# Optimization experiments

Hardware: AMD Instinct MI355X
Metric: run time of the kernel (lower is better)

## Reference

```python
import jax, jax.numpy as jnp
import numpy as np

# Straight-through binarization: forward hard threshold, backward identity.
# Matches BinarizeTensorThresh / BinarizedLinearFunction / BinaryActivation STE
# semantics from the diffnaps my_layers module (grad_weight = g^T x, i.e. the
# continuous weight receives the gradient of the binary weight unchanged).

def make_ste(thresh):
    @jax.custom_vjp
    def f(x):
        return (x >= thresh).astype(x.dtype)
    def fwd(x):
        return f(x), None
    def bwd(_, g):
        return (g,)
    f.defvjp(fwd, bwd)
    return f

ste_half = make_ste(0.5)  # weight binarization threshold (the 0.5 ctor arg)
ste_one = make_ste(1.0)   # activation fires when (pre-act + bias) >= 1

B, D, H, L = 4096, 5000, 2000, 50  # batch, input_dim(items), hidden_dim(patterns), label_dim
DATA_SPARSITY = 0.05


def setup_inputs() -> dict:
    key = jax.random.key(0)
    k = jax.random.split(key, 5)
    # sparse binary transaction data
    x = (jax.random.uniform(k[0], (B, D)) < DATA_SPARSITY).astype(jnp.float32)
    # continuous encoder weight in [0,1); binarized at 0.5 inside forward
    W_enc = jax.random.uniform(k[1], (H, D), dtype=jnp.float32)
    # small negative encoder bias (BinaPs-style init)
    b_enc = -jnp.abs(jax.random.normal(k[2], (H,), dtype=jnp.float32)) * 0.1
    act0_bias = jnp.zeros((H,), jnp.float32)
    act3_bias = jnp.zeros((D,), jnp.float32)
    # classifier_weight = logit(clip(N(0.1, 0.1), 0.01, 0.99)) as in __init__
    y = jnp.clip(0.1 + 0.1 * jax.random.normal(k[3], (L, H), dtype=jnp.float32), 0.01, 0.99)
    classifier_weight = jnp.log(y / (1.0 - y))
    return {
        "x": x,
        "W_enc": W_enc,
        "b_enc": b_enc,
        "act0_bias": act0_bias,
        "act3_bias": act3_bias,
        "classifier_weight": classifier_weight,
    }


def reference(x, W_enc, b_enc, act0_bias, act3_bias, classifier_weight):
    # fc0_enc: binarized-weight linear with bias
    Wb = ste_half(W_enc)                       # [H, D] in {0,1}
    h = x @ Wb.T + b_enc                       # [B, H]
    # act0: binary activation (threshold 1 on biased pre-activation)
    z = ste_one(h + act0_bias)                 # [B, H]
    # classify: sigmoid-gated classifier head (external_classifier=None / mode 'None')
    final_w = jax.nn.sigmoid(classifier_weight / 0.5)  # [L, H]
    classification = z @ final_w.T             # [B, L]
    # fc3_dec: shares the binarized encoder weight, transposed, no bias
    xd = z @ Wb                                # [B, D]
    output = ste_one(xd + act3_bias)           # [B, D]
    return output, classification, z
```

## Files before the change

kernel.cpp:

```cpp
#include <hip/hip_runtime.h>
#include <stdint.h>

static constexpr int Bn = 4096;
static constexpr int Dn = 5000;
static constexpr int Hn = 2000;
static constexpr int Ln = 50;
static constexpr int XW = 80;
static constexpr int Hpad = 2048;
static constexpr int Dpad = 5120;

typedef int v4i __attribute__((ext_vector_type(4)));
typedef int v16i __attribute__((ext_vector_type(16)));

#if defined(__has_builtin)
#if __has_builtin(__builtin_amdgcn_global_load_lds)
#define HAVE_GLOAD_LDS 1
#endif
#endif

#ifdef HAVE_GLOAD_LDS
__device__ __forceinline__ void gload16(const uint8_t* g, uint8_t* l) {
  __builtin_amdgcn_global_load_lds(
      (const __attribute__((address_space(1))) uint32_t*)g,
      (__attribute__((address_space(3))) uint32_t*)l, 16, 0, 0);
}
#endif

__device__ __forceinline__ int popc_acc(uint64_t v, int acc) {
  acc = __builtin_popcount((uint32_t)v) + acc;
  acc = __builtin_popcount((uint32_t)(v >> 32)) + acc;
  return acc;
}

__global__ void k_pack_i8(const float* __restrict__ src, uint8_t* __restrict__ dst,
                          int nrows_out, int nrows_valid, int ncols_src) {
  int g = (int)blockIdx.x * 256 + (int)threadIdx.x;
  int row = g / (Dpad / 4);
  int c4 = g - row * (Dpad / 4);
  if (row >= nrows_out) return;
  int col = c4 * 4;
  uchar4 o = make_uchar4(0, 0, 0, 0);
  if (row < nrows_valid && col + 3 < ncols_src) {
    const float4 v = *(const float4*)(src + (size_t)row * ncols_src + col);
    o.x = v.x >= 0.5f; o.y = v.y >= 0.5f; o.z = v.z >= 0.5f; o.w = v.w >= 0.5f;
  }
  *(uchar4*)(dst + (size_t)row * Dpad + col) = o;
}

__global__ __launch_bounds__(256) void k_pack_w_dual(const float* __restrict__ W,
                                                     uint8_t* __restrict__ wi8,
                                                     uint8_t* __restrict__ wtd) {
  int d = (int)blockIdx.x * 256 + (int)threadIdx.x;
  int j0 = (int)blockIdx.y * 64;
  bool dv = d < Dn;
  uint64_t colbits = 0;
  for (int r = 0; r < 64; ++r) {
    int j = j0 + r;
    float v = (j < Hn && dv) ? W[(size_t)j * Dn + d] : 0.0f;
    uint8_t bit = (v >= 0.5f) ? 1 : 0;
    wi8[(size_t)j * Dpad + d] = bit;
    colbits |= ((uint64_t)bit) << r;
  }
  uint8_t* dst = wtd + (size_t)d * Hpad + j0;
#pragma unroll
  for (int q = 0; q < 4; ++q) {
    uint32_t u[4];
#pragma unroll
    for (int s = 0; s < 4; ++s) {
      uint32_t nib = (uint32_t)((colbits >> (q * 16 + s * 4)) & 0xFull);
      u[s] = (nib & 1u) | (((nib >> 1) & 1u) << 8) | (((nib >> 2) & 1u) << 16) |
             (((nib >> 3) & 1u) << 24);
    }
    *(uint4*)(dst + q * 16) = make_uint4(u[0], u[1], u[2], u[3]);
  }
}

__global__ void k_pack_x(const float* __restrict__ x, uint64_t* __restrict__ xb2) {
  int g = (int)((blockIdx.x * blockDim.x + threadIdx.x) >> 6);
  int lane = (int)(threadIdx.x & 63);
  constexpr int nq = XW >> 2;
  int row = g / nq;
  int q = g - row * nq;
  if (row >= Bn) return;
  int w0 = q << 2;
  unsigned long long m[4];
#pragma unroll
  for (int e = 0; e < 4; ++e) {
    int col = ((w0 + e) << 6) + lane;
    float v = (col < Dn) ? x[(size_t)row * Dn + col] : 0.0f;
    m[e] = __ballot(v >= 0.5f);
  }
  if (lane < 4) {
    unsigned long long mv = m[0];
    mv = (lane == 1) ? m[1] : mv;
    mv = (lane == 2) ? m[2] : mv;
    mv = (lane == 3) ? m[3] : mv;
    int w = w0 + lane;
    xb2[((size_t)(w >> 1) * Bn + row) * 2 + (w & 1)] = mv;
  }
}

__global__ void k_pack_w(const float* __restrict__ W, uint64_t* __restrict__ wbT) {
  int g = (int)((blockIdx.x * blockDim.x + threadIdx.x) >> 6);
  int lane = (int)(threadIdx.x & 63);
  constexpr int nq = XW >> 2;
  int row = g / nq;
  int q = g - row * nq;
  if (row >= Hn) return;
  int w0 = q << 2;
  unsigned long long m[4];
#pragma unroll
  for (int e = 0; e < 4; ++e) {
    int col = ((w0 + e) << 6) + lane;
    float v = (col < Dn) ? W[(size_t)row * Dn + col] : 0.0f;
    m[e] = __ballot(v >= 0.5f);
  }
  if (lane < 4) {
    unsigned long long mv = m[0];
    mv = (lane == 1) ? m[1] : mv;
    mv = (lane == 2) ? m[2] : mv;
    mv = (lane == 3) ? m[3] : mv;
    wbT[(size_t)(w0 + lane) * Hpad + row] = mv;
  }
}

__global__ void k_transp(const uint64_t* __restrict__ wbT, uint32_t* __restrict__ wt32) {
  int g = (int)((blockIdx.x * blockDim.x + threadIdx.x) >> 6);
  int lane = (int)(threadIdx.x & 63);
  int w = g % XW;
  int jc = g / XW;
  if (jc >= Hpad / 64) return;
  uint64_t word = wbT[(size_t)w * Hpad + jc * 64 + lane];
  uint64_t mym = 0;
#pragma unroll
  for (int e = 0; e < 64; ++e) {
    unsigned long long m = __ballot((word >> e) & 1ull);
    mym = (lane == e) ? m : mym;
  }
  int d = w * 64 + lane;
  wt32[(size_t)(jc * 2) * Dpad + d] = (uint32_t)mym;
  wt32[(size_t)(jc * 2 + 1) * Dpad + d] = (uint32_t)(mym >> 32);
}

__global__ void k_pack_fwT(const float* __restrict__ cw, float* __restrict__ fwT) {
  int idx = blockIdx.x * blockDim.x + threadIdx.x;
  if (idx >= Hn * 64) return;
  int j = idx >> 6, l = idx & 63;
  float v = 0.0f;
  if (l < Ln) {
    float t = 2.0f * cw[(size_t)l * Hn + j];
    v = 1.0f / (1.0f + expf(-t));
  }
  fwT[idx] = v;
}

__global__ void k_zero(float* __restrict__ p, int n) {
  int i = blockIdx.x * blockDim.x + threadIdx.x;
  if (i < n) p[i] = 0.0f;
}


#ifdef HAVE_GLOAD_LDS
#define GEMM_PIPE(LDK, NT, Abase, Bbase)                                        \
  int srow_l = lane >> 2;                                           \
  int scol = (((lane & 3) ^ ((lane >> 3) & 3)) << 4);                          \
  const uint8_t* aSrc[2];                                                      \
  const uint8_t* bSrc[2];                                                      \
  uint8_t* asd[2][2];                                                          \
  uint8_t* bsd[2][2];                                                          \
  _Pragma("unroll") for (int i = 0; i < 2; ++i) {                              \
    int rbaseS = wv * 32 + i * 16;                                             \
    aSrc[i] = (Abase) + (size_t)(bm * 128 + rbaseS + srow_l) * (LDK) + scol;   \
    bSrc[i] = (Bbase) + (size_t)(bn * 128 + rbaseS + srow_l) * (LDK) + scol;   \
    asd[0][i] = As + rbaseS * 64;                                              \
    asd[1][i] = As + 8192 + rbaseS * 64;                                       \
    bsd[0][i] = Bs + rbaseS * 64;                                              \
    bsd[1][i] = Bs + 8192 + rbaseS * 64;                                       \
  }                                                                            \
  int arow = wm * 64 + (lane & 31);                                            \
  int brow = wn * 64 + (lane & 31);                                            \
  int khalf = lane >> 5;                                                       \
  int asl = (arow >> 1) & 3;                                                   \
  int bsl = (brow >> 1) & 3;                                                   \
                                                                 \
  _Pragma("unroll") for (int i = 0; i < 2; ++i) {                              \
    gload16(aSrc[i], asd[0][i]);                                               \
    gload16(bSrc[i], bsd[0][i]);                                               \
  }                                                                            \
  __syncthreads();                                                             \
  _Pragma("unroll 1") for (int t = 0; t < (NT); ++t) {                         \
    int cur = t & 1;                                                           \
    if (t + 1 < (NT)) {                                                        \
      size_t koff = (size_t)(t + 1) * 64;                                      \
      _Pragma("unroll") for (int i = 0; i < 2; ++i) {                          \
        gload16(aSrc[i] + koff, asd[cur ^ 1][i]);                              \
        gload16(bSrc[i] + koff, bsd[cur ^ 1][i]);                              \
      }                                                                        \
    }                                                                          \
    const uint8_t* Ab = As + cur * 8192;                                       \
    const uint8_t* Bb = Bs + cur * 8192;                                       \
    _Pragma("unroll") for (int kk = 0; kk < 2; ++kk) {                         \
      int kq = kk * 2 + khalf;                                                 \
      v4i a0 = *(const v4i*)(Ab + arow * 64 + ((kq ^ asl) << 4));              \
      v4i a1 = *(const v4i*)(Ab + (arow + 32) * 64 + ((kq ^ asl) << 4));       \
      v4i b0 = *(const v4i*)(Bb + brow * 64 + ((kq ^ bsl) << 4));              \
      v4i b1 = *(const v4i*)(Bb + (brow + 32) * 64 + ((kq ^ bsl) << 4));       \
      acc[0][0] = __builtin_amdgcn_mfma_i32_32x32x32_i8(a0, b0, acc[0][0], 0, 0, 0); \
      acc[0][1] = __builtin_amdgcn_mfma_i32_32x32x32_i8(a0, b1, acc[0][1], 0, 0, 0); \
      acc[1][0] = __builtin_amdgcn_mfma_i32_32x32x32_i8(a1, b0, acc[1][0], 0, 0, 0); \
      acc[1][1] = __builtin_amdgcn_mfma_i32_32x32x32_i8(a1, b1, acc[1][1], 0, 0, 0); \
    }                                                                          \
    __syncthreads();                                                           \
  }
#else
#define GEMM_PIPE(LDK, NT, Abase, Bbase)                                       \
  int srow_l = tid >> 2;                                            \
  int sq = tid & 3;                                                            \
  const uint8_t* ap0 = (Abase) + (size_t)(bm * 128 + srow_l) * (LDK) + sq * 16;\
  const uint8_t* ap1 = ap0 + (size_t)64 * (LDK);                               \
  const uint8_t* bp0 = (Bbase) + (size_t)(bn * 128 + srow_l) * (LDK) + sq * 16;\
  const uint8_t* bp1 = bp0 + (size_t)64 * (LDK);                               \
  int lw0 = srow_l * 64 + ((sq ^ ((srow_l >> 1) & 3)) << 4);                   \
  int lw1 = (64 + srow_l) * 64 + ((sq ^ (((64 + srow_l) >> 1) & 3)) << 4);     \
  int arow = wm * 64 + (lane & 31);                                            \
  int brow = wn * 64 + (lane & 31);                                            \
  int khalf = lane >> 5;                                                       \
  int asl = (arow >> 1) & 3;                                                   \
  int bsl = (brow >> 1) & 3;                                                   \
  _Pragma("unroll 1") for (int t = 0; t < (NT); ++t) {                         \
    size_t koff = (size_t)t * 64;                                              \
    v4i ra0 = *(const v4i*)(ap0 + koff);                                       \
    v4i ra1 = *(const v4i*)(ap1 + koff);                                       \
    v4i rb0 = *(const v4i*)(bp0 + koff);                                       \
    v4i rb1 = *(const v4i*)(bp1 + koff);                                       \
    __syncthreads();                                                           \
    *(v4i*)(As + lw0) = ra0;                                                   \
    *(v4i*)(As + lw1) = ra1;                                                   \
    *(v4i*)(Bs + lw0) = rb0;                                                   \
    *(v4i*)(Bs + lw1) = rb1;                                                   \
    __syncthreads();                                                           \
    _Pragma("unroll") for (int kk = 0; kk < 2; ++kk) {                         \
      int kq = kk * 2 + khalf;                                                 \
      v4i a0 = *(const v4i*)(As + arow * 64 + ((kq ^ asl) << 4));              \
      v4i a1 = *(const v4i*)(As + (arow + 32) * 64 + ((kq ^ asl) << 4));       \
      v4i b0 = *(const v4i*)(Bs + brow * 64 + ((kq ^ bsl) << 4));              \
      v4i b1 = *(const v4i*)(Bs + (brow + 32) * 64 + ((kq ^ bsl) << 4));       \
      acc[0][0] = __builtin_amdgcn_mfma_i32_32x32x32_i8(a0, b0, acc[0][0], 0, 0, 0); \
      acc[0][1] = __builtin_amdgcn_mfma_i32_32x32x32_i8(a0, b1, acc[0][1], 0, 0, 0); \
      acc[1][0] = __builtin_amdgcn_mfma_i32_32x32x32_i8(a1, b0, acc[1][0], 0, 0, 0); \
      acc[1][1] = __builtin_amdgcn_mfma_i32_32x32x32_i8(a1, b1, acc[1][1], 0, 0, 0); \
    }                                                                          \
  }
#endif

__global__ __launch_bounds__(256) void k_enc_mfma(
    const uint8_t* __restrict__ A, const uint8_t* __restrict__ B,
    const float* __restrict__ b_enc, const float* __restrict__ act0b,
    float* __restrict__ z_out, uint8_t* __restrict__ zi8) {
#ifdef HAVE_GLOAD_LDS
  __shared__ uint8_t As[2 * 128 * 64];
  __shared__ uint8_t Bs[2 * 128 * 64];
#else
  __shared__ uint8_t As[128 * 64];
  __shared__ uint8_t Bs[128 * 64];
#endif
  int tid = (int)threadIdx.x;
  int bn = (int)blockIdx.x;
  int bm = (int)blockIdx.y;
  int wv = __builtin_amdgcn_readfirstlane(tid >> 6);
  int lane = tid & 63;
  int wm = wv >> 1, wn = wv & 1;

  v16i acc[2][2];
#pragma unroll
  for (int i = 0; i < 2; ++i)
#pragma unroll
    for (int j = 0; j < 2; ++j) acc[i][j] = (v16i)0;

  GEMM_PIPE(Dpad, Dpad / 64, A, B)

  int col0 = bn * 128 + wn * 64 + (lane & 31);
#pragma unroll
  for (int ni = 0; ni < 2; ++ni) {
    int j = col0 + ni * 32;
    int js = (j < Hn) ? j : (Hn - 1);
    float be = b_enc[js];
    float ab = act0b[js];
    bool jv = j < Hn;
#pragma unroll
    for (int mi = 0; mi < 2; ++mi) {
      int rbase = bm * 128 + wm * 64 + mi * 32;
#pragma unroll
      for (int r = 0; r < 16; ++r) {
        int rloc = (r & 3) + 8 * (r >> 2) + 4 * (lane >> 5);
        int b = rbase + rloc;
        float h = ((float)acc[mi][ni][r] + be) + ab;
        bool zb = jv && (h >= 1.0f);
        if (jv) {
          z_out[(size_t)b * Hn + j] = zb ? 1.0f : 0.0f;
          zi8[(size_t)b * Hpad + j] = zb ? 1 : 0;
        }
      }
    }
  }
}

__global__ __launch_bounds__(256) void k_dec_mfma(
    const uint8_t* __restrict__ A,
    const uint8_t* __restrict__ B,
    const float* __restrict__ act3b, float* __restrict__ out) {
#ifdef HAVE_GLOAD_LDS
  __shared__ uint8_t As[2 * 128 * 64];
  __shared__ uint8_t Bs[2 * 128 * 64];
#else
  __shared__ uint8_t As[128 * 64];
  __shared__ uint8_t Bs[128 * 64];
#endif
  int tid = (int)threadIdx.x;
  int bn = (int)blockIdx.x;
  int bm = (int)blockIdx.y;
  int wv = __builtin_amdgcn_readfirstlane(tid >> 6);
  int lane = tid & 63;
  int wm = wv >> 1, wn = wv & 1;

  v16i acc[2][2];
#pragma unroll
  for (int i = 0; i < 2; ++i)
#pragma unroll
    for (int j = 0; j < 2; ++j) acc[i][j] = (v16i)0;

  GEMM_PIPE(Hpad, Hpad / 64, A, B)

  int col0 = bn * 128 + wn * 64 + (lane & 31);
#pragma unroll
  for (int ni = 0; ni < 2; ++ni) {
    int d = col0 + ni * 32;
    int ds = (d < Dn) ? d : (Dn - 1);
    float ab = act3b[ds];
    bool dv = d < Dn;
#pragma unroll
    for (int mi = 0; mi < 2; ++mi) {
      int rbase = bm * 128 + wm * 64 + mi * 32;
#pragma unroll
      for (int r = 0; r < 16; ++r) {
        int rloc = (r & 3) + 8 * (r >> 2) + 4 * (lane >> 5);
        int b = rbase + rloc;
        if (dv) out[(size_t)b * Dn + d] = (((float)acc[mi][ni][r] + ab) >= 1.0f) ? 1.0f : 0.0f;
      }
    }
  }
}

__global__ __launch_bounds__(256) void k_enc_bit(const uint64_t* __restrict__ xb2,
                                                 const uint64_t* __restrict__ wbT,
                                                 const float* __restrict__ b_enc,
                                                 const float* __restrict__ act0b,
                                                 float* __restrict__ z_out,
                                                 uint8_t* __restrict__ zb8) {
  __shared__ uint64_t wl[XW][8];
  int tid = (int)threadIdx.x;
  int jg = (int)blockIdx.x;
  int j0 = jg << 3;
#pragma unroll
  for (int k = 0; k < 3; ++k) {
    int idx = k * 256 + tid;
    if (idx < XW * 8) {
      int w = idx >> 3, j = idx & 7;
      wl[w][j] = wbT[(size_t)w * Hpad + j0 + j];
    }
  }
  __syncthreads();
  int wv = __builtin_amdgcn_readfirstlane(tid >> 6);
  int lane = tid & 63;
  int bg = (int)blockIdx.y * 4 + wv;
  int b0 = (bg << 8) + lane;
  int acc[4][8] = {};
  const uint64_t* xp = xb2 + 2 * (size_t)b0;
#pragma unroll 1
  for (int w2 = 0; w2 < XW / 2; ++w2) {
    ulong2 xx[4];
#pragma unroll
    for (int i = 0; i < 4; ++i)
      xx[i] = *(const ulong2*)(xp + ((size_t)w2 * Bn + i * 64) * 2);
#pragma unroll
    for (int t2 = 0; t2 < 4; ++t2) {
      ulong2 wa = *(ulong2*)&wl[2 * w2][2 * t2];
      ulong2 wb = *(ulong2*)&wl[2 * w2 + 1][2 * t2];
#pragma unroll
      for (int i = 0; i < 4; ++i) {
        acc[i][2 * t2]     = popc_acc(xx[i].x & wa.x, acc[i][2 * t2]);
        acc[i][2 * t2 + 1] = popc_acc(xx[i].x & wa.y, acc[i][2 * t2 + 1]);
        acc[i][2 * t2]     = popc_acc(xx[i].y & wb.x, acc[i][2 * t2]);
        acc[i][2 * t2 + 1] = popc_acc(xx[i].y & wb.y, acc[i][2 * t2 + 1]);
      }
    }
  }
  float be[8], ab[8];
#pragma unroll
  for (int t = 0; t < 8; ++t) {
    int j = j0 + t;
    int js = (j < Hn) ? j : (Hn - 1);
    be[t] = b_enc[js];
    ab[t] = act0b[js];
  }
#pragma unroll
  for (int i = 0; i < 4; ++i) {
    int b = b0 + i * 64;
    uint32_t zbyte = 0;
    float zf[8];
#pragma unroll
    for (int t = 0; t < 8; ++t) {
      int j = j0 + t;
      float h = ((float)acc[i][t] + be[t]) + ab[t];
      bool zb = (j < Hn) && (h >= 1.0f);
      zbyte |= zb ? (1u << t) : 0u;
      zf[t] = zb ? 1.0f : 0.0f;
    }
    zb8[((size_t)(jg >> 2) * Bn + b) * 4 + (jg & 3)] = (uint8_t)zbyte;
    if (j0 < Hn) {
      float* zp = z_out + (size_t)b * Hn + j0;
      *(float4*)zp = make_float4(zf[0], zf[1], zf[2], zf[3]);
      *(float4*)(zp + 4) = make_float4(zf[4], zf[5], zf[6], zf[7]);
    }
  }
}

__global__ __launch_bounds__(256, 6) void k_dec_bit(const uint32_t* __restrict__ zb32,
                                                    const uint32_t* __restrict__ wt32,
                                                    const float* __restrict__ act3b,
                                                    float* __restrict__ out) {
  __shared__ uint32_t tl[64][8];
  int tid = (int)threadIdx.x;
  int dc = (int)blockIdx.x;
  int d0 = dc << 3;
  {
#pragma unroll
    for (int k = 0; k < 2; ++k) {
      int e = k * 256 + tid;
      int hw = e >> 3, dl = e & 7;
      tl[hw][dl] = wt32[(size_t)hw * Dpad + d0 + dl];
    }
  }
  __syncthreads();
  int wv = __builtin_amdgcn_readfirstlane(tid >> 6);
  int lane = tid & 63;
  int bg = (int)blockIdx.y * 4 + wv;
  int b0 = (bg << 8) + lane;
  int acc[4][8] = {};
  const uint32_t* zp = zb32 + b0;
  uint32_t z0, z1, z2, z3, n0, n1, n2, n3;
  uint4 wA, wB, wAn, wBn;
  z0 = zp[0]; z1 = zp[64]; z2 = zp[128]; z3 = zp[192];
  wA = *(const uint4*)&tl[0][0];
  wB = *(const uint4*)&tl[0][4];
#define DEC_MAC()                                          \
  do {                                                     \
    acc[0][0] = __builtin_popcount(z0 & wA.x) + acc[0][0]; \
    acc[0][1] = __builtin_popcount(z0 & wA.y) + acc[0][1]; \
    acc[0][2] = __builtin_popcount(z0 & wA.z) + acc[0][2]; \
    acc[0][3] = __builtin_popcount(z0 & wA.w) + acc[0][3]; \
    acc[0][4] = __builtin_popcount(z0 & wB.x) + acc[0][4]; \
    acc[0][5] = __builtin_popcount(z0 & wB.y) + acc[0][5]; \
    acc[0][6] = __builtin_popcount(z0 & wB.z) + acc[0][6]; \
    acc[0][7] = __builtin_popcount(z0 & wB.w) + acc[0][7]; \
    acc[1][0] = __builtin_popcount(z1 & wA.x) + acc[1][0]; \
    acc[1][1] = __builtin_popcount(z1 & wA.y) + acc[1][1]; \
    acc[1][2] = __builtin_popcount(z1 & wA.z) + acc[1][2]; \
    acc[1][3] = __builtin_popcount(z1 & wA.w) + acc[1][3]; \
    acc[1][4] = __builtin_popcount(z1 & wB.x) + acc[1][4]; \
    acc[1][5] = __builtin_popcount(z1 & wB.y) + acc[1][5]; \
    acc[1][6] = __builtin_popcount(z1 & wB.z) + acc[1][6]; \
    acc[1][7] = __builtin_popcount(z1 & wB.w) + acc[1][7]; \
    acc[2][0] = __builtin_popcount(z2 & wA.x) + acc[2][0]; \
    acc[2][1] = __builtin_popcount(z2 & wA.y) + acc[2][1]; \
    acc[2][2] = __builtin_popcount(z2 & wA.z) + acc[2][2]; \
    acc[2][3] = __builtin_popcount(z2 & wA.w) + acc[2][3]; \
    acc[2][4] = __builtin_popcount(z2 & wB.x) + acc[2][4]; \
    acc[2][5] = __builtin_popcount(z2 & wB.y) + acc[2][5]; \
    acc[2][6] = __builtin_popcount(z2 & wB.z) + acc[2][6]; \
    acc[2][7] = __builtin_popcount(z2 & wB.w) + acc[2][7]; \
    acc[3][0] = __builtin_popcount(z3 & wA.x) + acc[3][0]; \
    acc[3][1] = __builtin_popcount(z3 & wA.y) + acc[3][1]; \
    acc[3][2] = __builtin_popcount(z3 & wA.z) + acc[3][2]; \
    acc[3][3] = __builtin_popcount(z3 & wA.w) + acc[3][3]; \
    acc[3][4] = __builtin_popcount(z3 & wB.x) + acc[3][4]; \
    acc[3][5] = __builtin_popcount(z3 & wB.y) + acc[3][5]; \
    acc[3][6] = __builtin_popcount(z3 & wB.z) + acc[3][6]; \
    acc[3][7] = __builtin_popcount(z3 & wB.w) + acc[3][7]; \
  } while (0)
#pragma unroll 1
  for (int hw = 0; hw < 64; ++hw) {
    int hn = (hw < 63) ? hw + 1 : hw;
    const uint32_t* zq = zp + (size_t)hn * Bn;
    n0 = zq[0]; n1 = zq[64]; n2 = zq[128]; n3 = zq[192];
    wAn = *(const uint4*)&tl[hn][0];
    wBn = *(const uint4*)&tl[hn][4];
    DEC_MAC();
    z0 = n0; z1 = n1; z2 = n2; z3 = n3;
    wA = wAn; wB = wBn;
  }
#undef DEC_MAC
  float ab[8];
#pragma unroll
  for (int t = 0; t < 8; ++t) {
    int d = d0 + t;
    int ds = (d < Dn) ? d : (Dn - 1);
    ab[t] = act3b[ds];
  }
  if (d0 < Dn) {
#pragma unroll
    for (int i = 0; i < 4; ++i) {
      int b = b0 + i * 64;
      float of[8];
#pragma unroll
      for (int t = 0; t < 8; ++t)
        of[t] = (((float)acc[i][t] + ab[t]) >= 1.0f) ? 1.0f : 0.0f;
      float* op = out + (size_t)b * Dn + d0;
      *(float4*)op = make_float4(of[0], of[1], of[2], of[3]);
      *(float4*)(op + 4) = make_float4(of[4], of[5], of[6], of[7]);
    }
  }
}

__global__ __launch_bounds__(256) void k_cls_i8(const uint8_t* __restrict__ zi8,
                                                const float* __restrict__ fwT,
                                                float* __restrict__ cls) {
  __shared__ float zT[64][132];
  __shared__ float fwL[64][64];
  int tid = (int)threadIdx.x;
  int bb0 = (int)blockIdx.x * 128;
  int jsp = (int)blockIdx.y;
  int tx = tid & 15, ty = tid >> 4;
  float acc[8][4] = {};
  for (int tile = 0; tile < 4; ++tile) {
    int jt0 = jsp * 256 + tile * 64;
    __syncthreads();
#pragma unroll
    for (int k = 0; k < 8; ++k) {
      int idx = k * 256 + tid;
      int r = idx >> 4, c4 = idx & 15;
      int j = jt0 + c4 * 4;
      uchar4 v = make_uchar4(0, 0, 0, 0);
      if (j < Hn) v = *(const uchar4*)(zi8 + (size_t)(bb0 + r) * Hpad + j);
      zT[c4 * 4 + 0][r] = (float)v.x;
      zT[c4 * 4 + 1][r] = (float)v.y;
      zT[c4 * 4 + 2][r] = (float)v.z;
      zT[c4 * 4 + 3][r] = (float)v.w;
    }
#pragma unroll
    for (int k = 0; k < 4; ++k) {
      int idx = k * 256 + tid;
      int jj = idx >> 4, c4 = idx & 15;
      int j = jt0 + jj;
      float4 v = make_float4(0.f, 0.f, 0.f, 0.f);
      if (j < Hn) v = *(const float4*)(fwT + (size_t)j * 64 + c4 * 4);
      *(float4*)&fwL[jj][c4 * 4] = v;
    }
    __syncthreads();
#pragma unroll 4
    for (int jj = 0; jj < 64; ++jj) {
      float4 fv = *(float4*)&fwL[jj][tx * 4];
      float4 za = *(float4*)&zT[jj][ty * 8];
      float4 zb = *(float4*)&zT[jj][ty * 8 + 4];
      float zz[8] = {za.x, za.y, za.z, za.w, zb.x, zb.y, zb.z, zb.w};
      float ff[4] = {fv.x, fv.y, fv.z, fv.w};
#pragma unroll
      for (int i = 0; i < 8; ++i)
#pragma unroll
        for (int l = 0; l < 4; ++l) acc[i][l] += zz[i] * ff[l];
    }
  }
#pragma unroll
  for (int i = 0; i < 8; ++i) {
    int b = bb0 + ty * 8 + i;
#pragma unroll
    for (int l = 0; l < 4; ++l) {
      int L = tx * 4 + l;
      if (L < Ln) atomicAdd(&cls[(size_t)b * Ln + L], acc[i][l]);
    }
  }
}

__global__ __launch_bounds__(256) void k_cls_f32(const float* __restrict__ z,
                                                 const float* __restrict__ fwT,
                                                 float* __restrict__ cls) {
  __shared__ float zT[64][132];
  __shared__ float fwL[64][64];
  int tid = (int)threadIdx.x;
  int bb0 = (int)blockIdx.x * 128;
  int jsp = (int)blockIdx.y;
  int tx = tid & 15, ty = tid >> 4;
  float acc[8][4] = {};
  for (int tile = 0; tile < 4; ++tile) {
    int jt0 = jsp * 256 + tile * 64;
    __syncthreads();
#pragma unroll
    for (int k = 0; k < 8; ++k) {
      int idx = k * 256 + tid;
      int r = idx >> 4, c4 = idx & 15;
      int j = jt0 + c4 * 4;
      float4 v = make_float4(0.f, 0.f, 0.f, 0.f);
      if (j < Hn) v = *(const float4*)(z + (size_t)(bb0 + r) * Hn + j);
      zT[c4 * 4 + 0][r] = v.x;
      zT[c4 * 4 + 1][r] = v.y;
      zT[c4 * 4 + 2][r] = v.z;
      zT[c4 * 4 + 3][r] = v.w;
    }
#pragma unroll
    for (int k = 0; k < 4; ++k) {
      int idx = k * 256 + tid;
      int jj = idx >> 4, c4 = idx & 15;
      int j = jt0 + jj;
      float4 v = make_float4(0.f, 0.f, 0.f, 0.f);
      if (j < Hn) v = *(const float4*)(fwT + (size_t)j * 64 + c4 * 4);
      *(float4*)&fwL[jj][c4 * 4] = v;
    }
    __syncthreads();
#pragma unroll 4
    for (int jj = 0; jj < 64; ++jj) {
      float4 fv = *(float4*)&fwL[jj][tx * 4];
      float4 za = *(float4*)&zT[jj][ty * 8];
      float4 zb = *(float4*)&zT[jj][ty * 8 + 4];
      float zz[8] = {za.x, za.y, za.z, za.w, zb.x, zb.y, zb.z, zb.w};
      float ff[4] = {fv.x, fv.y, fv.z, fv.w};
#pragma unroll
      for (int i = 0; i < 8; ++i)
#pragma unroll
        for (int l = 0; l < 4; ++l) acc[i][l] += zz[i] * ff[l];
    }
  }
#pragma unroll
  for (int i = 0; i < 8; ++i) {
    int b = bb0 + ty * 8 + i;
#pragma unroll
    for (int l = 0; l < 4; ++l) {
      int L = tx * 4 + l;
      if (L < Ln) atomicAdd(&cls[(size_t)b * Ln + L], acc[i][l]);
    }
  }
}

extern "C" void kernel_launch(void* const* d_in, const int* in_sizes, int n_in,
                              void* d_out, int out_size, void* d_ws, size_t ws_size,
                              hipStream_t stream) {
  const float* x     = (const float*)d_in[0];
  const float* W     = (const float*)d_in[1];
  const float* b_enc = (const float*)d_in[2];
  const float* act0b = (const float*)d_in[3];
  const float* act3b = (const float*)d_in[4];
  const float* cw    = (const float*)d_in[5];

  float* out0 = (float*)d_out;
  float* cls  = out0 + (size_t)Bn * Dn;
  float* zout = cls + (size_t)Bn * Ln;

  char* p = (char*)d_ws;
  uint32_t* zb32 = (uint32_t*)p; p += (size_t)64 * Bn * 4;
  float*    fwT  = (float*)p;    p += (size_t)Hn * 64 * 4;
  size_t common = (size_t)(p - (char*)d_ws);

  size_t sz_xi8 = (size_t)Bn * Dpad;
  size_t sz_wi8 = (size_t)Hpad * Dpad;
  size_t sz_zi8 = (size_t)Bn * Hpad;
  size_t sz_wtd = (size_t)Dpad * Hpad;
  size_t sz_wbT = (size_t)XW * Hpad * 8;
  size_t sz_wt32 = (size_t)64 * Dpad * 4;
  size_t full_need = common + sz_xi8 + sz_wi8 + sz_zi8 + sz_wtd;

  k_pack_fwT<<<(Hn * 64 + 255) / 256, 256, 0, stream>>>(cw, fwT);
  k_zero<<<(Bn * Ln + 255) / 256, 256, 0, stream>>>(cls, Bn * Ln);

  if (ws_size >= full_need) {
    uint8_t* xi8 = (uint8_t*)p;
    uint8_t* wi8 = xi8 + sz_xi8;
    uint8_t* zi8 = wi8 + sz_wi8;
    uint8_t* wtd = zi8 + sz_zi8;
    k_pack_i8<<<(Bn * (Dpad / 4) + 255) / 256, 256, 0, stream>>>(x, xi8, Bn, Bn, Dn);
    dim3 gwd(Dpad / 256, Hpad / 64);
    k_pack_w_dual<<<gwd, 256, 0, stream>>>(W, wi8, wtd);
    dim3 ge(Hpad / 128, Bn / 128);
    k_enc_mfma<<<ge, 256, 0, stream>>>(xi8, wi8, b_enc, act0b, zout, zi8);
    dim3 g3(32, 8);
    k_cls_i8<<<g3, 256, 0, stream>>>(zi8, fwT, cls);
    dim3 gd(Dpad / 128, Bn / 128);
    k_dec_mfma<<<gd, 256, 0, stream>>>(zi8, wtd, act3b, out0);
  } else {
    uint64_t* wbT  = (uint64_t*)p;
    uint32_t* wt32 = (uint32_t*)(p + sz_wbT);
    uint64_t* xb2  = (uint64_t*)(p + sz_wbT + sz_wt32);
    {
      long long waves = (long long)Hn * (XW / 4);
      k_pack_w<<<(int)((waves * 64 + 255) / 256), 256, 0, stream>>>(W, wbT);
    }
    {
      long long waves = (long long)(Hpad / 64) * XW;
      k_transp<<<(int)((waves * 64 + 255) / 256), 256, 0, stream>>>(wbT, wt32);
    }
    {
      long long waves = (long long)Bn * (XW / 4);
      k_pack_x<<<(int)((waves * 64 + 255) / 256), 256, 0, stream>>>(x, xb2);
    }
    dim3 g1(256, 4);
    k_enc_bit<<<g1, 256, 0, stream>>>(xb2, wbT, b_enc, act0b, zout, (uint8_t*)zb32);
    dim3 g3(32, 8);
    k_cls_f32<<<g3, 256, 0, stream>>>(zout, fwT, cls);
    dim3 g2(640, 4);
    k_dec_bit<<<g2, 256, 0, stream>>>(zb32, wt32, act3b, out0);
  }
}
```

Before: 246.0 us.

## Store int8 operands in k-blocked 16-byte layout and deepen GEMM k-tile to 128

```diff
diff --git a/kernel.cpp b/kernel.cpp
--- a/kernel.cpp
+++ b/kernel.cpp
@@ -32,36 +32,47 @@
   return acc;
 }
 
-__global__ void k_pack_i8(const float* __restrict__ src, uint8_t* __restrict__ dst,
-                          int nrows_out, int nrows_valid, int ncols_src) {
+__global__ void k_pack_xT(const float* __restrict__ x, uint8_t* __restrict__ xiT) {
   int g = (int)blockIdx.x * 256 + (int)threadIdx.x;
-  int row = g / (Dpad / 4);
-  int c4 = g - row * (Dpad / 4);
-  if (row >= nrows_out) return;
-  int col = c4 * 4;
-  uchar4 o = make_uchar4(0, 0, 0, 0);
-  if (row < nrows_valid && col + 3 < ncols_src) {
-    const float4 v = *(const float4*)(src + (size_t)row * ncols_src + col);
-    o.x = v.x >= 0.5f; o.y = v.y >= 0.5f; o.z = v.z >= 0.5f; o.w = v.w >= 0.5f;
-  }
-  *(uchar4*)(dst + (size_t)row * Dpad + col) = o;
-}
-
-__global__ __launch_bounds__(256) void k_pack_w_dual(const float* __restrict__ W,
-                                                     uint8_t* __restrict__ wi8,
-                                                     uint8_t* __restrict__ wtd) {
+  int kb = g >> 12;
+  int row = g & 4095;
+  if (kb >= Dpad / 16) return;
+  uint8_t o[16];
+  int c0 = kb * 16;
+  if (c0 + 15 < Dn) {
+#pragma unroll
+    for (int q = 0; q < 4; ++q) {
+      float4 v = *(const float4*)(x + (size_t)row * Dn + c0 + q * 4);
+      o[q * 4 + 0] = v.x >= 0.5f;
+      o[q * 4 + 1] = v.y >= 0.5f;
+      o[q * 4 + 2] = v.z >= 0.5f;
+      o[q * 4 + 3] = v.w >= 0.5f;
+    }
+  } else {
+#pragma unroll
+    for (int e = 0; e < 16; ++e) {
+      int c = c0 + e;
+      o[e] = (c < Dn) ? (x[(size_t)row * Dn + c] >= 0.5f ? 1 : 0) : 0;
+    }
+  }
+  *(uint4*)(xiT + ((size_t)kb * Bn + row) * 16) = *(uint4*)o;
+}
+
+__global__ __launch_bounds__(256) void k_pack_w_dualT(const float* __restrict__ W,
+                                                      uint8_t* __restrict__ wi8T,
+                                                      uint8_t* __restrict__ wtdT) {
   int d = (int)blockIdx.x * 256 + (int)threadIdx.x;
   int j0 = (int)blockIdx.y * 64;
   bool dv = d < Dn;
+  int dc = d >> 4, de = d & 15;
   uint64_t colbits = 0;
   for (int r = 0; r < 64; ++r) {
     int j = j0 + r;
     float v = (j < Hn && dv) ? W[(size_t)j * Dn + d] : 0.0f;
     uint8_t bit = (v >= 0.5f) ? 1 : 0;
-    wi8[(size_t)j * Dpad + d] = bit;
+    wi8T[((size_t)dc * Hpad + j) * 16 + de] = bit;
     colbits |= ((uint64_t)bit) << r;
   }
-  uint8_t* dst = wtd + (size_t)d * Hpad + j0;
 #pragma unroll
   for (int q = 0; q < 4; ++q) {
     uint32_t u[4];
@@ -71,7 +82,8 @@
       u[s] = (nib & 1u) | (((nib >> 1) & 1u) << 8) | (((nib >> 2) & 1u) << 16) |
              (((nib >> 3) & 1u) << 24);
     }
-    *(uint4*)(dst + q * 16) = make_uint4(u[0], u[1], u[2], u[3]);
+    *(uint4*)(wtdT + (((size_t)(j0 >> 4) + q) * Dpad + d) * 16) =
+        make_uint4(u[0], u[1], u[2], u[3]);
   }
 }
 
@@ -161,50 +173,42 @@
 
 
 #ifdef HAVE_GLOAD_LDS
-#define GEMM_PIPE(LDK, NT, Abase, Bbase)                                        \
-  int srow_l = lane >> 2;                                           \
-  int scol = (((lane & 3) ^ ((lane >> 3) & 3)) << 4);                          \
-  const uint8_t* aSrc[2];                                                      \
-  const uint8_t* bSrc[2];                                                      \
-  uint8_t* asd[2][2];                                                          \
-  uint8_t* bsd[2][2];                                                          \
+#define GEMM_PIPE(AROWS, BROWS, NT, Abase, Bbase)                               \
+  const uint8_t* aS = (Abase) + ((size_t)bm * 128 + lane) * 16;                \
+  const uint8_t* bS = (Bbase) + ((size_t)bn * 128 + lane) * 16;                \
+  int kqw = 2 * wv;                           \
   _Pragma("unroll") for (int i = 0; i < 2; ++i) {                              \
-    int rbaseS = wv * 32 + i * 16;                                             \
-    aSrc[i] = (Abase) + (size_t)(bm * 128 + rbaseS + srow_l) * (LDK) + scol;   \
-    bSrc[i] = (Bbase) + (size_t)(bn * 128 + rbaseS + srow_l) * (LDK) + scol;   \
-    asd[0][i] = As + rbaseS * 64;                                              \
-    asd[1][i] = As + 8192 + rbaseS * 64;                                       \
-    bsd[0][i] = Bs + rbaseS * 64;                                              \
-    bsd[1][i] = Bs + 8192 + rbaseS * 64;                                       \
+    _Pragma("unroll") for (int c = 0; c < 2; ++c) {                            \
+      gload16(aS + ((size_t)(kqw + i) * (AROWS) + c * 64) * 16,                \
+              As + (kqw + i) * 2048 + c * 1024);                               \
+      gload16(bS + ((size_t)(kqw + i) * (BROWS) + c * 64) * 16,                \
+              Bs + (kqw + i) * 2048 + c * 1024);                               \
+    }                                                                          \
   }                                                                            \
+  __syncthreads();                                                             \
   int arow = wm * 64 + (lane & 31);                                            \
   int brow = wn * 64 + (lane & 31);                                            \
   int khalf = lane >> 5;                                                       \
-  int asl = (arow >> 1) & 3;                                                   \
-  int bsl = (brow >> 1) & 3;                                                   \
-                                                                 \
-  _Pragma("unroll") for (int i = 0; i < 2; ++i) {                              \
-    gload16(aSrc[i], asd[0][i]);                                               \
-    gload16(bSrc[i], bsd[0][i]);                                               \
-  }                                                                            \
-  __syncthreads();                                                             \
   _Pragma("unroll 1") for (int t = 0; t < (NT); ++t) {                         \
     int cur = t & 1;                                                           \
     if (t + 1 < (NT)) {                                                        \
-      size_t koff = (size_t)(t + 1) * 64;                                      \
+      size_t kb8 = (size_t)(t + 1) * 8;                                        \
       _Pragma("unroll") for (int i = 0; i < 2; ++i) {                          \
-        gload16(aSrc[i] + koff, asd[cur ^ 1][i]);                              \
-        gload16(bSrc[i] + koff, bsd[cur ^ 1][i]);                              \
+        _Pragma("unroll") for (int c = 0; c < 2; ++c) {                        \
+          gload16(aS + ((kb8 + kqw + i) * (AROWS) + c * 64) * 16,              \
+                  As + (cur ^ 1) * 16384 + (kqw + i) * 2048 + c * 1024);       \
+          gload16(bS + ((kb8 + kqw + i) * (BROWS) + c * 64) * 16,              \
+                  Bs + (cur ^ 1) * 16384 + (kqw + i) * 2048 + c * 1024);       \
+        }                                                                      \
       }                                                                        \
     }                                                                          \
-    const uint8_t* Ab = As + cur * 8192;                                       \
-    const uint8_t* Bb = Bs + cur * 8192;                                       \
-    _Pragma("unroll") for (int kk = 0; kk < 2; ++kk) {                         \
-      int kq = kk * 2 + khalf;                                                 \
-      v4i a0 = *(const v4i*)(Ab + arow * 64 + ((kq ^ asl) << 4));              \
-      v4i a1 = *(const v4i*)(Ab + (arow + 32) * 64 + ((kq ^ asl) << 4));       \
-      v4i b0 = *(const v4i*)(Bb + brow * 64 + ((kq ^ bsl) << 4));              \
-      v4i b1 = *(const v4i*)(Bb + (brow + 32) * 64 + ((kq ^ bsl) << 4));       \
+    const uint8_t* Ab = As + cur * 16384 + khalf * 2048;                       \
+    const uint8_t* Bb = Bs + cur * 16384 + khalf * 2048;                       \
+    _Pragma("unroll") for (int kk = 0; kk < 4; ++kk) {                         \
+      v4i a0 = *(const v4i*)(Ab + kk * 4096 + arow * 16);                      \
+      v4i a1 = *(const v4i*)(Ab + kk * 4096 + (arow + 32) * 16);               \
+      v4i b0 = *(const v4i*)(Bb + kk * 4096 + brow * 16);                      \
+      v4i b1 = *(const v4i*)(Bb + kk * 4096 + (brow + 32) * 16);               \
       acc[0][0] = __builtin_amdgcn_mfma_i32_32x32x32_i8(a0, b0, acc[0][0], 0, 0, 0); \
       acc[0][1] = __builtin_amdgcn_mfma_i32_32x32x32_i8(a0, b1, acc[0][1], 0, 0, 0); \
       acc[1][0] = __builtin_amdgcn_mfma_i32_32x32x32_i8(a1, b0, acc[1][0], 0, 0, 0); \
@@ -213,56 +217,51 @@
     __syncthreads();                                                           \
   }
 #else
-#define GEMM_PIPE(LDK, NT, Abase, Bbase)                                       \
-  int srow_l = tid >> 2;                                            \
-  int sq = tid & 3;                                                            \
-  const uint8_t* ap0 = (Abase) + (size_t)(bm * 128 + srow_l) * (LDK) + sq * 16;\
-  const uint8_t* ap1 = ap0 + (size_t)64 * (LDK);                               \
-  const uint8_t* bp0 = (Bbase) + (size_t)(bn * 128 + srow_l) * (LDK) + sq * 16;\
-  const uint8_t* bp1 = bp0 + (size_t)64 * (LDK);                               \
-  int lw0 = srow_l * 64 + ((sq ^ ((srow_l >> 1) & 3)) << 4);                   \
-  int lw1 = (64 + srow_l) * 64 + ((sq ^ (((64 + srow_l) >> 1) & 3)) << 4);     \
+#define GEMM_PIPE(AROWS, BROWS, NT, Abase, Bbase)                              \
+  int skq = tid >> 5;                                                          \
+  int sr4 = (tid & 31) * 4;                                                    \
   int arow = wm * 64 + (lane & 31);                                            \
   int brow = wn * 64 + (lane & 31);                                            \
   int khalf = lane >> 5;                                                       \
-  int asl = (arow >> 1) & 3;                                                   \
-  int bsl = (brow >> 1) & 3;                                                   \
   _Pragma("unroll 1") for (int t = 0; t < (NT); ++t) {                         \
-    size_t koff = (size_t)t * 64;                                              \
-    v4i ra0 = *(const v4i*)(ap0 + koff);                                       \
-    v4i ra1 = *(const v4i*)(ap1 + koff);                                       \
-    v4i rb0 = *(const v4i*)(bp0 + koff);                                       \
-    v4i rb1 = *(const v4i*)(bp1 + koff);                                       \
+    size_t kb = (size_t)t * 8 + skq;                                           \
+    v4i ra[4], rb[4];                                                          \
+    _Pragma("unroll") for (int i = 0; i < 4; ++i) {                            \
+      ra[i] = *(const v4i*)((Abase) + (kb * (AROWS) + bm * 128 + sr4 + i) * 16); \
+      rb[i] = *(const v4i*)((Bbase) + (kb * (BROWS) + bn * 128 + sr4 + i) * 16); \
+    }                                                                          \
     __syncthreads();                                                           \
-    *(v4i*)(As + lw0) = ra0;                                                   \
-    *(v4i*)(As + lw1) = ra1;                                                   \
-    *(v4i*)(Bs + lw0) = rb0;                                                   \
-    *(v4i*)(Bs + lw1) = rb1;                                                   \
+    _Pragma("unroll") for (int i = 0; i < 4; ++i) {                            \
+      *(v4i*)(As + skq * 2048 + (sr4 + i) * 16) = ra[i];                       \
+      *(v4i*)(Bs + skq * 2048 + (sr4 + i) * 16) = rb[i];                       \
+    }                                                                          \
     __syncthreads();                                                           \
-    _Pragma("unroll") for (int kk = 0; kk < 2; ++kk) {                         \
-      int kq = kk * 2 + khalf;                                                 \
-      v4i a0 = *(const v4i*)(As + arow * 64 + ((kq ^ asl) << 4));              \
-      v4i a1 = *(const v4i*)(As + (arow + 32) * 64 + ((kq ^ asl) << 4));       \
-      v4i b0 = *(const v4i*)(Bs + brow * 64 + ((kq ^ bsl) << 4));              \
-      v4i b1 = *(const v4i*)(Bs + (brow + 32) * 64 + ((kq ^ bsl) << 4));       \
+    _Pragma("unroll") for (int kk = 0; kk < 4; ++kk) {                         \
+      const uint8_t* Ab = As + (kk * 2 + khalf) * 2048;                        \
+      const uint8_t* Bb = Bs + (kk * 2 + khalf) * 2048;                        \
+      v4i a0 = *(const v4i*)(Ab + arow * 16);                                  \
+      v4i a1 = *(const v4i*)(Ab + (arow + 32) * 16);                           \
+      v4i b0 = *(const v4i*)(Bb + brow * 16);                                  \
+      v4i b1 = *(const v4i*)(Bb + (brow + 32) * 16);                           \
       acc[0][0] = __builtin_amdgcn_mfma_i32_32x32x32_i8(a0, b0, acc[0][0], 0, 0, 0); \
       acc[0][1] = __builtin_amdgcn_mfma_i32_32x32x32_i8(a0, b1, acc[0][1], 0, 0, 0); \
       acc[1][0] = __builtin_amdgcn_mfma_i32_32x32x32_i8(a1, b0, acc[1][0], 0, 0, 0); \
       acc[1][1] = __builtin_amdgcn_mfma_i32_32x32x32_i8(a1, b1, acc[1][1], 0, 0, 0); \
     }                                                                          \
+    __syncthreads();                                                           \
   }
 #endif
 
 __global__ __launch_bounds__(256) void k_enc_mfma(
     const uint8_t* __restrict__ A, const uint8_t* __restrict__ B,
     const float* __restrict__ b_enc, const float* __restrict__ act0b,
-    float* __restrict__ z_out, uint8_t* __restrict__ zi8) {
+    float* __restrict__ z_out, uint8_t* __restrict__ zi8T) {
 #ifdef HAVE_GLOAD_LDS
-  __shared__ uint8_t As[2 * 128 * 64];
-  __shared__ uint8_t Bs[2 * 128 * 64];
+  __shared__ uint8_t As[2 * 16384];
+  __shared__ uint8_t Bs[2 * 16384];
 #else
-  __shared__ uint8_t As[128 * 64];
-  __shared__ uint8_t Bs[128 * 64];
+  __shared__ uint8_t As[16384];
+  __shared__ uint8_t Bs[16384];
 #endif
   int tid = (int)threadIdx.x;
   int bn = (int)blockIdx.x;
@@ -277,7 +276,7 @@
 #pragma unroll
     for (int j = 0; j < 2; ++j) acc[i][j] = (v16i)0;
 
-  GEMM_PIPE(Dpad, Dpad / 64, A, B)
+  GEMM_PIPE(Bn, Hpad, Dpad / 128, A, B)
 
   int col0 = bn * 128 + wn * 64 + (lane & 31);
 #pragma unroll
@@ -298,7 +297,7 @@
         bool zb = jv && (h >= 1.0f);
         if (jv) {
           z_out[(size_t)b * Hn + j] = zb ? 1.0f : 0.0f;
-          zi8[(size_t)b * Hpad + j] = zb ? 1 : 0;
+          zi8T[((size_t)(j >> 4) * Bn + b) * 16 + (j & 15)] = zb ? 1 : 0;
         }
       }
     }
@@ -310,11 +309,11 @@
     const uint8_t* __restrict__ B,
     const float* __restrict__ act3b, float* __restrict__ out) {
 #ifdef HAVE_GLOAD_LDS
-  __shared__ uint8_t As[2 * 128 * 64];
-  __shared__ uint8_t Bs[2 * 128 * 64];
+  __shared__ uint8_t As[2 * 16384];
+  __shared__ uint8_t Bs[2 * 16384];
 #else
-  __shared__ uint8_t As[128 * 64];
-  __shared__ uint8_t Bs[128 * 64];
+  __shared__ uint8_t As[16384];
+  __shared__ uint8_t Bs[16384];
 #endif
   int tid = (int)threadIdx.x;
   int bn = (int)blockIdx.x;
@@ -329,7 +328,7 @@
 #pragma unroll
     for (int j = 0; j < 2; ++j) acc[i][j] = (v16i)0;
 
-  GEMM_PIPE(Hpad, Hpad / 64, A, B)
+  GEMM_PIPE(Bn, Dpad, Hpad / 128, A, B)
 
   int col0 = bn * 128 + wn * 64 + (lane & 31);
 #pragma unroll
@@ -522,7 +521,7 @@
   }
 }
 
-__global__ __launch_bounds__(256) void k_cls_i8(const uint8_t* __restrict__ zi8,
+__global__ __launch_bounds__(256) void k_cls_i8(const uint8_t* __restrict__ zi8T,
                                                 const float* __restrict__ fwT,
                                                 float* __restrict__ cls) {
   __shared__ float zT[64][132];
@@ -541,7 +540,8 @@
       int r = idx >> 4, c4 = idx & 15;
       int j = jt0 + c4 * 4;
       uchar4 v = make_uchar4(0, 0, 0, 0);
-      if (j < Hn) v = *(const uchar4*)(zi8 + (size_t)(bb0 + r) * Hpad + j);
+      if (j < Hn)
+        v = *(const uchar4*)(zi8T + ((size_t)(j >> 4) * Bn + (bb0 + r)) * 16 + (j & 15));
       zT[c4 * 4 + 0][r] = (float)v.x;
       zT[c4 * 4 + 1][r] = (float)v.y;
       zT[c4 * 4 + 2][r] = (float)v.z;
@@ -671,19 +671,19 @@
   k_zero<<<(Bn * Ln + 255) / 256, 256, 0, stream>>>(cls, Bn * Ln);
 
   if (ws_size >= full_need) {
-    uint8_t* xi8 = (uint8_t*)p;
-    uint8_t* wi8 = xi8 + sz_xi8;
-    uint8_t* zi8 = wi8 + sz_wi8;
-    uint8_t* wtd = zi8 + sz_zi8;
-    k_pack_i8<<<(Bn * (Dpad / 4) + 255) / 256, 256, 0, stream>>>(x, xi8, Bn, Bn, Dn);
+    uint8_t* xiT  = (uint8_t*)p;
+    uint8_t* wi8T = xiT + sz_xi8;
+    uint8_t* zi8T = wi8T + sz_wi8;
+    uint8_t* wtdT = zi8T + sz_zi8;
+    k_pack_xT<<<(Dpad / 16) * Bn / 256, 256, 0, stream>>>(x, xiT);
     dim3 gwd(Dpad / 256, Hpad / 64);
-    k_pack_w_dual<<<gwd, 256, 0, stream>>>(W, wi8, wtd);
+    k_pack_w_dualT<<<gwd, 256, 0, stream>>>(W, wi8T, wtdT);
     dim3 ge(Hpad / 128, Bn / 128);
-    k_enc_mfma<<<ge, 256, 0, stream>>>(xi8, wi8, b_enc, act0b, zout, zi8);
+    k_enc_mfma<<<ge, 256, 0, stream>>>(xiT, wi8T, b_enc, act0b, zout, zi8T);
     dim3 g3(32, 8);
-    k_cls_i8<<<g3, 256, 0, stream>>>(zi8, fwT, cls);
+    k_cls_i8<<<g3, 256, 0, stream>>>(zi8T, fwT, cls);
     dim3 gd(Dpad / 128, Bn / 128);
-    k_dec_mfma<<<gd, 256, 0, stream>>>(zi8, wtd, act3b, out0);
+    k_dec_mfma<<<gd, 256, 0, stream>>>(zi8T, wtdT, act3b, out0);
   } else {
     uint64_t* wbT  = (uint64_t*)p;
     uint32_t* wt32 = (uint32_t*)(p + sz_wbT);
```

After: 238.4 us. 3.1% less time.
